# Kernel tuning notes

Measured on AMD Instinct MI355X. Metric: run time of the kernel, lower is better.

Reference implementation:

```python
import jax, jax.numpy as jnp
import numpy as np

V, D, H, L, T_CTX = 50257, 768, 12, 12, 1024
HD = D // H
GELU_C = float(np.sqrt(2.0 / np.pi))


def new_gelu(x):
    return 0.5 * x * (1.0 + jnp.tanh(GELU_C * (x + 0.044715 * x ** 3)))


def layernorm(x, w, b, eps=1e-5):
    mu = jnp.mean(x, axis=-1, keepdims=True)
    var = jnp.var(x, axis=-1, keepdims=True)
    return (x - mu) * jax.lax.rsqrt(var + eps) * w + b


def setup_inputs() -> dict:
    key = jax.random.key(0)
    ks = jax.random.split(key, 20)
    B, T = 2, 1024
    s = 0.02
    inp = {
        "idx": jax.random.randint(ks[0], (B, T), 0, V),
        "targets": jax.random.randint(ks[1], (B, T), 0, V),
        "wte": jax.random.normal(ks[2], (V, D), jnp.float32) * s,
        "wpe": jax.random.normal(ks[3], (T_CTX, D), jnp.float32) * s,
        "ln1_w": jnp.ones((L, D)), "ln1_b": jnp.zeros((L, D)),
        "qkv_w": jax.random.normal(ks[4], (L, D, 3 * D), jnp.float32) * s,
        "qkv_b": jnp.zeros((L, 3 * D)),
        "proj_w": jax.random.normal(ks[5], (L, D, D), jnp.float32) * s,
        "proj_b": jnp.zeros((L, D)),
        "ln2_w": jnp.ones((L, D)), "ln2_b": jnp.zeros((L, D)),
        "fc_w": jax.random.normal(ks[6], (L, D, 4 * D), jnp.float32) * s,
        "fc_b": jnp.zeros((L, 4 * D)),
        "fc2_w": jax.random.normal(ks[7], (L, 4 * D, D), jnp.float32) * s,
        "fc2_b": jnp.zeros((L, D)),
        "lnf_w": jnp.ones((D,)), "lnf_b": jnp.zeros((D,)),
    }
    return inp


def _gpt_forward(idx, targets, wte, wpe, ln1_w, ln1_b, qkv_w, qkv_b, proj_w,
                 proj_b, ln2_w, ln2_b, fc_w, fc_b, fc2_w, fc2_b, lnf_w, lnf_b):
    B, T = idx.shape
    x = wte[idx] + wpe[:T]  # [B,T,D]
    scale = 1.0 / np.sqrt(HD)
    causal = jnp.tril(jnp.ones((T, T), dtype=bool))

    def block(x, p):
        l1w, l1b, qw, qb, pw, pb, l2w, l2b, fw, fb, f2w, f2b = p
        h = layernorm(x, l1w, l1b)
        qkv = h @ qw + qb  # [B,T,3D]
        q, k, v = jnp.split(qkv, 3, axis=-1)
        q = q.reshape(B, T, H, HD).transpose(0, 2, 1, 3)
        k = k.reshape(B, T, H, HD).transpose(0, 2, 1, 3)
        v = v.reshape(B, T, H, HD).transpose(0, 2, 1, 3)
        attn = jnp.einsum('bhqd,bhkd->bhqk', q, k) * scale
        attn = jnp.where(causal, attn, -jnp.inf)
        attn = jax.nn.softmax(attn, axis=-1)
        o = jnp.einsum('bhqk,bhkd->bhqd', attn, v)
        o = o.transpose(0, 2, 1, 3).reshape(B, T, D)
        x = x + (o @ pw + pb)
        h = layernorm(x, l2w, l2b)
        h = new_gelu(h @ fw + fb) @ f2w + f2b
        return x + h, None

    params = (ln1_w, ln1_b, qkv_w, qkv_b, proj_w, proj_b,
              ln2_w, ln2_b, fc_w, fc_b, fc2_w, fc2_b)
    x, _ = jax.lax.scan(block, x, params)
    x = layernorm(x, lnf_w, lnf_b)
    logits = x @ wte.T  # tied lm_head, [B,T,V]

    logp = jax.nn.log_softmax(logits, axis=-1)
    tflat = targets.reshape(-1)
    valid = tflat != -1
    tsafe = jnp.where(valid, tflat, 0)
    nll = -jnp.take_along_axis(logp.reshape(-1, V), tsafe[:, None], axis=-1)[:, 0]
    loss = jnp.sum(jnp.where(valid, nll, 0.0)) / jnp.maximum(jnp.sum(valid), 1)
    return logits, loss


def reference(idx, targets, wte, wpe, ln1_w, ln1_b, qkv_w, qkv_b, proj_w,
              proj_b, ln2_w, ln2_b, fc_w, fc_b, fc2_w, fc2_b, lnf_w, lnf_b):
    return _gpt_forward(idx, targets, wte, wpe, ln1_w, ln1_b, qkv_w, qkv_b,
                        proj_w, proj_b, ln2_w, ln2_b, fc_w, fc_b, fc2_w, fc2_b,
                        lnf_w, lnf_b)
```

## Files before the change

kernel.cpp:

```cpp
#include <hip/hip_runtime.h>
#include <hip/hip_bf16.h>
#include <math.h>

#define TT 1024
#define BB 2
#define DD 768
#define HH 12
#define NHD 64
#define LL 12
#define VV 50257
#define MROWS (BB*TT)
#define VPAD 50304

typedef __attribute__((ext_vector_type(4))) float f32x4;
typedef __attribute__((ext_vector_type(8))) __bf16 bf16x8;
typedef __attribute__((ext_vector_type(8))) unsigned short u16x8;
typedef __hip_bfloat16 bf16;

__device__ __forceinline__ void gload_lds16(const bf16* g, bf16* l) {
    __builtin_amdgcn_global_load_lds((const __attribute__((address_space(1))) void*)g,
                                     (__attribute__((address_space(3))) void*)l, 16, 0, 0);
}

__global__ void embed_kernel(const int* __restrict__ idx, const float* __restrict__ wte,
                             const float* __restrict__ wpe, float* __restrict__ x) {
    int m = blockIdx.x;
    int t = m % TT;
    int tok = idx[m];
    const float* wrow = wte + (size_t)tok * DD;
    const float* prow = wpe + (size_t)t * DD;
    float* xrow = x + (size_t)m * DD;
    for (int c = threadIdx.x; c < DD; c += blockDim.x)
        xrow[c] = wrow[c] + prow[c];
}

__global__ void ln_kernel(const float* __restrict__ x, const float* __restrict__ w,
                          const float* __restrict__ b, bf16* __restrict__ out) {
    __shared__ float red[256];
    int m = blockIdx.x;
    int tid = threadIdx.x;
    const float* xr = x + (size_t)m * DD;
    float v0 = xr[tid], v1 = xr[tid + 256], v2 = xr[tid + 512];
    red[tid] = v0 + v1 + v2;
    __syncthreads();
    for (int s = 128; s > 0; s >>= 1) { if (tid < s) red[tid] += red[tid + s]; __syncthreads(); }
    float mu = red[0] * (1.0f / DD);
    __syncthreads();
    float d0 = v0 - mu, d1 = v1 - mu, d2 = v2 - mu;
    red[tid] = d0 * d0 + d1 * d1 + d2 * d2;
    __syncthreads();
    for (int s = 128; s > 0; s >>= 1) { if (tid < s) red[tid] += red[tid + s]; __syncthreads(); }
    float rstd = rsqrtf(red[0] * (1.0f / DD) + 1e-5f);
    bf16* orow = out + (size_t)m * DD;
    orow[tid]       = __float2bfloat16(d0 * rstd * w[tid]       + b[tid]);
    orow[tid + 256] = __float2bfloat16(d1 * rstd * w[tid + 256] + b[tid + 256]);
    orow[tid + 512] = __float2bfloat16(d2 * rstd * w[tid + 512] + b[tid + 512]);
}

__global__ void cast_kernel(const float* __restrict__ src, bf16* __restrict__ dst, int n4) {
    int stride = gridDim.x * blockDim.x;
    for (int i = blockIdx.x * blockDim.x + threadIdx.x; i < n4; i += stride) {
        float4 v = *(const float4*)(src + (size_t)i * 4);
        bf16* d = dst + (size_t)i * 4;
        d[0] = __float2bfloat16(v.x); d[1] = __float2bfloat16(v.y);
        d[2] = __float2bfloat16(v.z); d[3] = __float2bfloat16(v.w);
    }
}

__global__ void tcast_kernel(const float* __restrict__ W, bf16* __restrict__ Wt,
                             int K, int N, size_t wstride, size_t tstride) {
    W  += (size_t)blockIdx.z * wstride;
    Wt += (size_t)blockIdx.z * tstride;
    __shared__ float t[32][33];
    int n0 = blockIdx.x * 32, k0 = blockIdx.y * 32;
    int c = threadIdx.x & 31, g = threadIdx.x >> 5;
    #pragma unroll
    for (int i = 0; i < 4; ++i) {
        int k = g * 4 + i;
        t[k][c] = W[(size_t)(k0 + k) * N + n0 + c];
    }
    __syncthreads();
    #pragma unroll
    for (int i = 0; i < 4; ++i) {
        int n = g * 4 + i;
        Wt[(size_t)(n0 + n) * K + k0 + c] = __float2bfloat16(t[c][n]);
    }
}

template<int BM, int BN, bool BIAS, bool GELU_, bool RES, bool OUTBF16, bool NCHECK, bool SPLITK>
__global__ __launch_bounds__(256, 3) void mgemm(
        const bf16* __restrict__ A, const bf16* __restrict__ Bm,
        const float* __restrict__ bias, const float* __restrict__ res,
        float* __restrict__ Cf, bf16* __restrict__ Cb, int M, int N, int K) {
    constexpr int WM = BM / 32, WN = BN / 32;
    constexpr int RA = BM / 64, RB = BN / 64;
    constexpr int NL = RA + RB;
    __shared__ __align__(16) bf16 As[2][BM * 32];
    __shared__ __align__(16) bf16 Bs[2][BN * 32];
    const int tid = threadIdx.x, lane = tid & 63, wid = tid >> 6;
    const int nbx = gridDim.x;
    const int nwg = nbx * gridDim.y;
    const int bidl = blockIdx.x + nbx * blockIdx.y;
    const int cpx = nwg >> 3;
    const int sw = (bidl & 7) * cpx + (bidl >> 3);
    const int m0 = (sw % nbx) * BM, n0 = (sw / nbx) * BN;
    const int wr = (wid >> 1) * (BM / 2), wc = (wid & 1) * (BN / 2);
    const int fr = lane & 15, fq = lane >> 4;

    const int Keff  = SPLITK ? (K >> 1) : K;
    const int kbase = SPLITK ? blockIdx.z * Keff : 0;
    if (SPLITK) Cf += (size_t)blockIdx.z * M * N;

    const int ksrc = ((lane & 3) ^ ((lane >> 3) & 3)) * 8;
    const bf16* gA = A  + (size_t)(m0 + wid * 16 + (lane >> 2)) * K + kbase + ksrc;
    const bf16* gB = Bm + (size_t)(n0 + wid * 16 + (lane >> 2)) * K + kbase + ksrc;
    bf16* lA = &As[0][0] + wid * 512 + lane * 8;
    bf16* lB = &Bs[0][0] + wid * 512 + lane * 8;
    const int kph = (fq ^ ((fr >> 1) & 3)) * 8;

    f32x4 acc[WM][WN] = {};
    const int nt = Keff / 32;

    #pragma unroll
    for (int i = 0; i < RA; ++i) gload_lds16(gA + (size_t)(i * 64) * K, lA + i * 2048);
    #pragma unroll
    for (int i = 0; i < RB; ++i) gload_lds16(gB + (size_t)(i * 64) * K, lB + i * 2048);

    for (int t = 0; t < nt; ++t) {
        const int cur = t & 1;
        if (t + 1 < nt) {
            const bf16* pA = gA + (t + 1) * 32;
            const bf16* pB = gB + (t + 1) * 32;
            bf16* dA = lA + (cur ^ 1) * (BM * 32);
            bf16* dB = lB + (cur ^ 1) * (BN * 32);
            #pragma unroll
            for (int i = 0; i < RA; ++i) gload_lds16(pA + (size_t)(i * 64) * K, dA + i * 2048);
            #pragma unroll
            for (int i = 0; i < RB; ++i) gload_lds16(pB + (size_t)(i * 64) * K, dB + i * 2048);
            asm volatile("s_waitcnt vmcnt(%0)" :: "i"(NL) : "memory");
        } else {
            asm volatile("s_waitcnt vmcnt(0)" ::: "memory");
        }
        __builtin_amdgcn_s_barrier();
        __builtin_amdgcn_sched_barrier(0);
        const bf16* abase = &As[cur][0];
        const bf16* bbase = &Bs[cur][0];
        bf16x8 af[WM], bq[WN];
        #pragma unroll
        for (int m = 0; m < WM; ++m)
            af[m] = *(const bf16x8*)(abase + (wr + m * 16 + fr) * 32 + kph);
        #pragma unroll
        for (int n = 0; n < WN; ++n)
            bq[n] = *(const bf16x8*)(bbase + (wc + n * 16 + fr) * 32 + kph);
        #pragma unroll
        for (int m = 0; m < WM; ++m)
            #pragma unroll
            for (int n = 0; n < WN; ++n)
                acc[m][n] = __builtin_amdgcn_mfma_f32_16x16x32_bf16(af[m], bq[n], acc[m][n], 0, 0, 0);
        __builtin_amdgcn_sched_barrier(0);
        __builtin_amdgcn_s_barrier();
    }

    #pragma unroll
    for (int m = 0; m < WM; ++m) {
        const int row = m0 + wr + m * 16 + fq * 4;
        #pragma unroll
        for (int n = 0; n < WN; ++n) {
            const int col = n0 + wc + n * 16 + fr;
            if (NCHECK && col >= N) continue;
            float bv = BIAS ? bias[col] : 0.f;
            #pragma unroll
            for (int r = 0; r < 4; ++r) {
                float v = acc[m][n][r] + bv;
                if (GELU_) {
                    float u = v;
                    v = 0.5f * u * (1.0f + tanhf(0.7978845608028654f * (u + 0.044715f * u * u * u)));
                }
                if (RES) v += res[(size_t)(row + r) * N + col];
                if (OUTBF16) Cb[(size_t)(row + r) * N + col] = __float2bfloat16(v);
                else         Cf[(size_t)(row + r) * N + col] = v;
            }
        }
    }
}

__global__ void red_kernel(const float* __restrict__ part, const float* __restrict__ bias,
                           float* __restrict__ x) {
    const size_t MN = (size_t)MROWS * DD;
    size_t i = ((size_t)blockIdx.x * blockDim.x + threadIdx.x) * 4;
    float4 p0 = *(const float4*)(part + i);
    float4 p1 = *(const float4*)(part + MN + i);
    float4 xv = *(const float4*)(x + i);
    float4 bv = *(const float4*)(bias + (int)(i % DD));
    xv.x += p0.x + p1.x + bv.x;
    xv.y += p0.y + p1.y + bv.y;
    xv.z += p0.z + p1.z + bv.z;
    xv.w += p0.w + p1.w + bv.w;
    *(float4*)(x + i) = xv;
}

__global__ __launch_bounds__(256) void attn3_kernel(const bf16* __restrict__ qkv,
                                                    bf16* __restrict__ out) {
    __shared__ bf16 Vt[64 * 64];
    __shared__ bf16 Ps[4][16 * 64];
    const int bid = blockIdx.x;
    const int q0 = (15 - (bid & 15)) * 64;
    const int h  = (bid / (TT / 64)) % HH;
    const int b  = bid / ((TT / 64) * HH);
    const int tid = threadIdx.x, lane = tid & 63, wid = tid >> 6;
    const int fr = lane & 15, fq = lane >> 4;
    const size_t rs = 3 * DD;

    bf16x8 qf[2];
    {
        const bf16* qb = qkv + (size_t)(b * TT + q0 + wid * 16 + fr) * rs + h * NHD;
        qf[0] = *(const bf16x8*)(qb + fq * 8);
        qf[1] = *(const bf16x8*)(qb + 32 + fq * 8);
    }
    float mrun[4] = {-1e30f, -1e30f, -1e30f, -1e30f};
    float lrun[4] = {0.f, 0.f, 0.f, 0.f};
    f32x4 o[4] = {};
    const int vrow = (tid & 31) * 2, kq = tid >> 5;
    const int ntile = q0 / 64 + 1;

    for (int jt = 0; jt < ntile; ++jt) {
        __syncthreads();
        {
            const u16x8* vb = (const u16x8*)(qkv + (size_t)(b * TT + jt * 64 + vrow) * rs + 2 * DD + h * NHD + kq * 8);
            u16x8 v0 = vb[0];
            u16x8 v1 = *(const u16x8*)((const bf16*)vb + rs);
            #pragma unroll
            for (int j = 0; j < 8; ++j) {
                int d = kq * 8 + j;
                int e = (d * 64 + vrow) ^ ((d & 7) << 3);
                *(unsigned int*)&Vt[e] = (unsigned int)v0[j] | ((unsigned int)v1[j] << 16);
            }
        }
        f32x4 s[4] = {};
        const bf16* kb = qkv + (size_t)(b * TT + jt * 64 + fr) * rs + DD + h * NHD;
        __builtin_amdgcn_s_setprio(1);
        #pragma unroll
        for (int n = 0; n < 4; ++n) {
            bf16x8 k0 = *(const bf16x8*)(kb + (size_t)(n * 16) * rs + fq * 8);
            bf16x8 k1 = *(const bf16x8*)(kb + (size_t)(n * 16) * rs + 32 + fq * 8);
            s[n] = __builtin_amdgcn_mfma_f32_16x16x32_bf16(qf[0], k0, s[n], 0, 0, 0);
            s[n] = __builtin_amdgcn_mfma_f32_16x16x32_bf16(qf[1], k1, s[n], 0, 0, 0);
        }
        __builtin_amdgcn_s_setprio(0);
        float mt[4] = {-1e30f, -1e30f, -1e30f, -1e30f};
        #pragma unroll
        for (int n = 0; n < 4; ++n) {
            int colg = jt * 64 + n * 16 + fr;
            #pragma unroll
            for (int r = 0; r < 4; ++r) {
                int rowg = q0 + wid * 16 + fq * 4 + r;
                float v = s[n][r] * 0.125f;
                if (colg > rowg) v = -1e30f;
                s[n][r] = v;
                mt[r] = fmaxf(mt[r], v);
            }
        }
        #pragma unroll
        for (int msk = 1; msk <= 8; msk <<= 1)
            #pragma unroll
            for (int r = 0; r < 4; ++r) mt[r] = fmaxf(mt[r], __shfl_xor(mt[r], msk));
        float sc[4], pt[4] = {0.f, 0.f, 0.f, 0.f};
        #pragma unroll
        for (int r = 0; r < 4; ++r) {
            float mn = fmaxf(mrun[r], mt[r]);
            sc[r] = __expf(mrun[r] - mn);
            mrun[r] = mn;
        }
        #pragma unroll
        for (int n = 0; n < 4; ++n)
            #pragma unroll
            for (int r = 0; r < 4; ++r) {
                float p = __expf(s[n][r] - mrun[r]);
                s[n][r] = p;
                pt[r] += p;
            }
        #pragma unroll
        for (int msk = 1; msk <= 8; msk <<= 1)
            #pragma unroll
            for (int r = 0; r < 4; ++r) pt[r] += __shfl_xor(pt[r], msk);
        #pragma unroll
        for (int r = 0; r < 4; ++r) lrun[r] = lrun[r] * sc[r] + pt[r];
        #pragma unroll
        for (int n2 = 0; n2 < 4; ++n2)
            #pragma unroll
            for (int r = 0; r < 4; ++r) o[n2][r] *= sc[r];
        #pragma unroll
        for (int n = 0; n < 4; ++n)
            #pragma unroll
            for (int r = 0; r < 4; ++r) {
                int row = fq * 4 + r;
                int e = (row * 64 + n * 16 + fr) ^ ((row & 7) << 3);
                Ps[wid][e] = __float2bfloat16(s[n][r]);
            }
        __syncthreads();
        __builtin_amdgcn_s_setprio(1);
        #pragma unroll
        for (int ks = 0; ks < 2; ++ks) {
            int pe = (fr * 64 + ks * 32 + fq * 8) ^ ((fr & 7) << 3);
            bf16x8 pa = *(const bf16x8*)&Ps[wid][pe];
            #pragma unroll
            for (int n2 = 0; n2 < 4; ++n2) {
                int d = n2 * 16 + fr;
                int ve = (d * 64 + ks * 32 + fq * 8) ^ ((d & 7) << 3);
                bf16x8 vv = *(const bf16x8*)&Vt[ve];
                o[n2] = __builtin_amdgcn_mfma_f32_16x16x32_bf16(pa, vv, o[n2], 0, 0, 0);
            }
        }
        __builtin_amdgcn_s_setprio(0);
    }
    #pragma unroll
    for (int r = 0; r < 4; ++r) {
        float inv = 1.f / lrun[r];
        bf16* op = out + (size_t)(b * TT + q0 + wid * 16 + fq * 4 + r) * DD + h * NHD;
        #pragma unroll
        for (int n2 = 0; n2 < 4; ++n2)
            op[n2 * 16 + fr] = __float2bfloat16(o[n2][r] * inv);
    }
}

__global__ void zero_kernel(float* p) { if (threadIdx.x == 0) p[0] = 0.f; }

__device__ __forceinline__ void ol_push(float v, float& mx, float& sm) {
    if (v > mx) { sm *= __expf(mx - v); mx = v; }
    sm += __expf(v - mx);
}

__global__ void loss_kernel(const float* __restrict__ logits, const int* __restrict__ targets,
                            float* __restrict__ acc) {
    __shared__ float rm[256], rs[256];
    int m = blockIdx.x;
    int tid = threadIdx.x;
    const float* lr = logits + (size_t)m * VV;
    const int lead = (4 - (m & 3)) & 3;
    const int nv = (VV - lead) >> 2;
    float mx = -1e30f, sm = 0.f;
    if (tid < lead) ol_push(lr[tid], mx, sm);
    const float4* lr4 = (const float4*)(lr + lead);
    for (int i = tid; i < nv; i += 256) {
        float4 v = lr4[i];
        ol_push(v.x, mx, sm); ol_push(v.y, mx, sm);
        ol_push(v.z, mx, sm); ol_push(v.w, mx, sm);
    }
    for (int i = lead + 4 * nv + tid; i < VV; i += 256) ol_push(lr[i], mx, sm);
    rm[tid] = mx; rs[tid] = sm;
    __syncthreads();
    for (int s = 128; s > 0; s >>= 1) {
        if (tid < s) {
            float m2 = rm[tid + s], s2 = rs[tid + s];
            float nm = fmaxf(rm[tid], m2);
            rs[tid] = rs[tid] * __expf(rm[tid] - nm) + s2 * __expf(m2 - nm);
            rm[tid] = nm;
        }
        __syncthreads();
    }
    if (tid == 0) {
        float lse = logf(rs[0]) + rm[0];
        atomicAdd(acc, lse - lr[targets[m]]);
    }
}

__global__ void loss_final(const float* __restrict__ acc, float* __restrict__ out) {
    if (threadIdx.x == 0) out[0] = acc[0] * (1.0f / (float)MROWS);
}

extern "C" void kernel_launch(void* const* d_in, const int* in_sizes, int n_in,
                              void* d_out, int out_size, void* d_ws, size_t ws_size,
                              hipStream_t stream) {
    const int*   idx     = (const int*)d_in[0];
    const int*   targets = (const int*)d_in[1];
    const float* wte     = (const float*)d_in[2];
    const float* wpe     = (const float*)d_in[3];
    const float* ln1_w   = (const float*)d_in[4];
    const float* ln1_b   = (const float*)d_in[5];
    const float* qkv_w   = (const float*)d_in[6];
    const float* qkv_b   = (const float*)d_in[7];
    const float* proj_w  = (const float*)d_in[8];
    const float* proj_b  = (const float*)d_in[9];
    const float* ln2_w   = (const float*)d_in[10];
    const float* ln2_b   = (const float*)d_in[11];
    const float* fc_w    = (const float*)d_in[12];
    const float* fc_b    = (const float*)d_in[13];
    const float* fc2_w   = (const float*)d_in[14];
    const float* fc2_b   = (const float*)d_in[15];
    const float* lnf_w   = (const float*)d_in[16];
    const float* lnf_b   = (const float*)d_in[17];

    float* logits = (float*)d_out;
    float* loss_out = logits + (size_t)MROWS * VV;

    const size_t LQ = (size_t)3 * DD * DD, LP = (size_t)DD * DD;
    const size_t LF = (size_t)4 * DD * DD, LF2 = (size_t)4 * DD * DD;
    const size_t LSTRIDE = LQ + LP + LF + LF2;

    float* x    = (float*)d_ws;
    float* lacc = x + (size_t)MROWS * DD;
    float* part = lacc + 16;
    bf16* qkvbuf = (bf16*)(part + (size_t)2 * MROWS * DD);
    bf16* hb   = qkvbuf + (size_t)MROWS * 3 * DD;
    bf16* ab   = hb + (size_t)MROWS * DD;
    bf16* gb   = ab + (size_t)MROWS * DD;
    bf16* wteb = gb + (size_t)MROWS * 4 * DD;
    bf16* wbase = wteb + (size_t)VPAD * DD;

    const size_t fixed_bytes = (size_t)((char*)wbase - (char*)d_ws);
    const bool hoist = ws_size >= fixed_bytes + sizeof(bf16) * LSTRIDE * LL;

    dim3 blk(256);
    cast_kernel<<<2048, blk, 0, stream>>>(wte, wteb, VV * DD / 4);
    embed_kernel<<<MROWS, blk, 0, stream>>>(idx, wte, wpe, x);

    if (hoist) {
        tcast_kernel<<<dim3(3 * DD / 32, DD / 32, LL), blk, 0, stream>>>(
            qkv_w, wbase, DD, 3 * DD, LQ, LSTRIDE);
        tcast_kernel<<<dim3(DD / 32, DD / 32, LL), blk, 0, stream>>>(
            proj_w, wbase + LQ, DD, DD, LP, LSTRIDE);
        tcast_kernel<<<dim3(4 * DD / 32, DD / 32, LL), blk, 0, stream>>>(
            fc_w, wbase + LQ + LP, DD, 4 * DD, LF, LSTRIDE);
        tcast_kernel<<<dim3(DD / 32, 4 * DD / 32, LL), blk, 0, stream>>>(
            fc2_w, wbase + LQ + LP + LF, 4 * DD, DD, LF2, LSTRIDE);
    }

    const int nred = (MROWS * DD) / (4 * 256);

    for (int l = 0; l < LL; ++l) {
        bf16* wl = hoist ? wbase + (size_t)l * LSTRIDE : wbase;
        bf16* wQT = wl, *wPT = wl + LQ, *wFT = wl + LQ + LP, *wF2T = wl + LQ + LP + LF;
        if (!hoist) {
            tcast_kernel<<<dim3(3 * DD / 32, DD / 32, 1), blk, 0, stream>>>(qkv_w + (size_t)l * LQ, wQT, DD, 3 * DD, 0, 0);
            tcast_kernel<<<dim3(DD / 32, DD / 32, 1), blk, 0, stream>>>(proj_w + (size_t)l * LP, wPT, DD, DD, 0, 0);
            tcast_kernel<<<dim3(4 * DD / 32, DD / 32, 1), blk, 0, stream>>>(fc_w + (size_t)l * LF, wFT, DD, 4 * DD, 0, 0);
            tcast_kernel<<<dim3(DD / 32, 4 * DD / 32, 1), blk, 0, stream>>>(fc2_w + (size_t)l * LF2, wF2T, 4 * DD, DD, 0, 0);
        }

        ln_kernel<<<MROWS, blk, 0, stream>>>(x, ln1_w + (size_t)l * DD, ln1_b + (size_t)l * DD, hb);

        mgemm<128, 128, true, false, false, true, false, false><<<dim3(MROWS / 128, 3 * DD / 128), blk, 0, stream>>>(
            hb, wQT, qkv_b + (size_t)l * 3 * DD, nullptr, nullptr, qkvbuf, MROWS, 3 * DD, DD);

        attn3_kernel<<<BB * HH * (TT / 64), blk, 0, stream>>>(qkvbuf, ab);

        mgemm<64, 64, false, false, false, false, false, true><<<dim3(MROWS / 64, DD / 64, 2), blk, 0, stream>>>(
            ab, wPT, nullptr, nullptr, part, nullptr, MROWS, DD, DD);
        red_kernel<<<nred, blk, 0, stream>>>(part, proj_b + (size_t)l * DD, x);

        ln_kernel<<<MROWS, blk, 0, stream>>>(x, ln2_w + (size_t)l * DD, ln2_b + (size_t)l * DD, hb);

        mgemm<128, 128, true, true, false, true, false, false><<<dim3(MROWS / 128, 4 * DD / 128), blk, 0, stream>>>(
            hb, wFT, fc_b + (size_t)l * 4 * DD, nullptr, nullptr, gb, MROWS, 4 * DD, DD);

        mgemm<64, 64, false, false, false, false, false, true><<<dim3(MROWS / 64, DD / 64, 2), blk, 0, stream>>>(
            gb, wF2T, nullptr, nullptr, part, nullptr, MROWS, DD, 4 * DD);
        red_kernel<<<nred, blk, 0, stream>>>(part, fc2_b + (size_t)l * DD, x);
    }

    ln_kernel<<<MROWS, blk, 0, stream>>>(x, lnf_w, lnf_b, hb);

    mgemm<128, 128, false, false, false, false, true, false><<<dim3(MROWS / 128, VPAD / 128), blk, 0, stream>>>(
        hb, wteb, nullptr, nullptr, logits, nullptr, MROWS, VV, DD);

    zero_kernel<<<1, 64, 0, stream>>>(lacc);
    loss_kernel<<<MROWS, blk, 0, stream>>>(logits, targets, lacc);
    loss_final<<<1, 64, 0, stream>>>(lacc, loss_out);
}
```

Before: 2.567 ms.

## Fuse residual reduction with layernorm, fuse logsumexp into lm_head GEMM, retune tiles

Merges the split-K reduction and residual add with the following layernorm into one redln kernel, removing separate ln/red launches and one pass over x. Adds a dedicated lm_head GEMM that writes logits with nontemporal stores and emits per-tile (max, sumexp) partials, so the loss kernel no longer rereads the full 2048x50257 logits. It also zero-pads the padded wte rows so the N check can be dropped, rewrites GELU as x*sigmoid(2z) using __expf, and changes the QKV and FC tile shapes. The result is more launches-saved fusion in exchange for extra code and slightly different GELU rounding.

After: 2.508 ms. 1.02x faster.

```diff
diff --git a/kernel.cpp b/kernel.cpp
--- a/kernel.cpp
+++ b/kernel.cpp
@@ -11,6 +11,7 @@
 #define VV 50257
 #define MROWS (BB*TT)
 #define VPAD 50304
+#define NT 393
 
 typedef __attribute__((ext_vector_type(4))) float f32x4;
 typedef __attribute__((ext_vector_type(8))) __bf16 bf16x8;
@@ -57,6 +58,37 @@
     orow[tid + 512] = __float2bfloat16(d2 * rstd * w[tid + 512] + b[tid + 512]);
 }
 
+__global__ void redln_kernel(const float* __restrict__ part, const float* __restrict__ bias,
+                             const float* __restrict__ w, const float* __restrict__ b,
+                             float* __restrict__ x, bf16* __restrict__ hb) {
+    __shared__ float red[256];
+    const size_t MN = (size_t)MROWS * DD;
+    int m = blockIdx.x;
+    int tid = threadIdx.x;
+    float v[3];
+    #pragma unroll
+    for (int j = 0; j < 3; ++j) {
+        int c = tid + j * 256;
+        size_t i = (size_t)m * DD + c;
+        v[j] = x[i] + part[i] + part[MN + i] + bias[c];
+        x[i] = v[j];
+    }
+    red[tid] = v[0] + v[1] + v[2];
+    __syncthreads();
+    for (int s = 128; s > 0; s >>= 1) { if (tid < s) red[tid] += red[tid + s]; __syncthreads(); }
+    float mu = red[0] * (1.0f / DD);
+    __syncthreads();
+    float d0 = v[0] - mu, d1 = v[1] - mu, d2 = v[2] - mu;
+    red[tid] = d0 * d0 + d1 * d1 + d2 * d2;
+    __syncthreads();
+    for (int s = 128; s > 0; s >>= 1) { if (tid < s) red[tid] += red[tid + s]; __syncthreads(); }
+    float rstd = rsqrtf(red[0] * (1.0f / DD) + 1e-5f);
+    bf16* orow = hb + (size_t)m * DD;
+    orow[tid]       = __float2bfloat16(d0 * rstd * w[tid]       + b[tid]);
+    orow[tid + 256] = __float2bfloat16(d1 * rstd * w[tid + 256] + b[tid + 256]);
+    orow[tid + 512] = __float2bfloat16(d2 * rstd * w[tid + 512] + b[tid + 512]);
+}
+
 __global__ void cast_kernel(const float* __restrict__ src, bf16* __restrict__ dst, int n4) {
     int stride = gridDim.x * blockDim.x;
     for (int i = blockIdx.x * blockDim.x + threadIdx.x; i < n4; i += stride) {
@@ -67,6 +99,11 @@
     }
 }
 
+__global__ void padzero_kernel(bf16* __restrict__ p, int n) {
+    int i = blockIdx.x * 256 + threadIdx.x;
+    if (i < n) p[i] = __float2bfloat16(0.f);
+}
+
 __global__ void tcast_kernel(const float* __restrict__ W, bf16* __restrict__ Wt,
                              int K, int N, size_t wstride, size_t tstride) {
     W  += (size_t)blockIdx.z * wstride;
@@ -87,7 +124,7 @@
     }
 }
 
-template<int BM, int BN, bool BIAS, bool GELU_, bool RES, bool OUTBF16, bool NCHECK, bool SPLITK>
+template<int BM, int BN, bool BIAS, bool GELU_, bool RES, bool OUTBF16, bool SPLITK>
 __global__ __launch_bounds__(256, 3) void mgemm(
         const bf16* __restrict__ A, const bf16* __restrict__ Bm,
         const float* __restrict__ bias, const float* __restrict__ res,
@@ -167,14 +204,14 @@
         #pragma unroll
         for (int n = 0; n < WN; ++n) {
             const int col = n0 + wc + n * 16 + fr;
-            if (NCHECK && col >= N) continue;
             float bv = BIAS ? bias[col] : 0.f;
             #pragma unroll
             for (int r = 0; r < 4; ++r) {
                 float v = acc[m][n][r] + bv;
                 if (GELU_) {
                     float u = v;
-                    v = 0.5f * u * (1.0f + tanhf(0.7978845608028654f * (u + 0.044715f * u * u * u)));
+                    float z = 1.5957691216057308f * (u + 0.044715f * u * u * u);
+                    v = u / (1.0f + __expf(-z));
                 }
                 if (RES) v += res[(size_t)(row + r) * N + col];
                 if (OUTBF16) Cb[(size_t)(row + r) * N + col] = __float2bfloat16(v);
@@ -184,20 +221,120 @@
     }
 }
 
-__global__ void red_kernel(const float* __restrict__ part, const float* __restrict__ bias,
-                           float* __restrict__ x) {
-    const size_t MN = (size_t)MROWS * DD;
-    size_t i = ((size_t)blockIdx.x * blockDim.x + threadIdx.x) * 4;
-    float4 p0 = *(const float4*)(part + i);
-    float4 p1 = *(const float4*)(part + MN + i);
-    float4 xv = *(const float4*)(x + i);
-    float4 bv = *(const float4*)(bias + (int)(i % DD));
-    xv.x += p0.x + p1.x + bv.x;
-    xv.y += p0.y + p1.y + bv.y;
-    xv.z += p0.z + p1.z + bv.z;
-    xv.w += p0.w + p1.w + bv.w;
-    *(float4*)(x + i) = xv;
-}
+__global__ __launch_bounds__(256, 3) void mgemmL(
+        const bf16* __restrict__ A, const bf16* __restrict__ Bm,
+        float* __restrict__ Cf, float2* __restrict__ P, int N, int K) {
+    constexpr int NL = 4;
+    __shared__ __align__(16) bf16 As[2][128 * 32];
+    __shared__ __align__(16) bf16 Bs[2][128 * 32];
+    __shared__ float2 lbuf[4][64];
+    const int tid = threadIdx.x, lane = tid & 63, wid = tid >> 6;
+    const int nbx = gridDim.x;
+    const int nwg = nbx * gridDim.y;
+    const int bidl = blockIdx.x + nbx * blockIdx.y;
+    const int cpx = nwg >> 3;
+    const int sw = (bidl & 7) * cpx + (bidl >> 3);
+    const int m0 = (sw % nbx) * 128, n0 = (sw / nbx) * 128;
+    const int wr = (wid >> 1) * 64, wc = (wid & 1) * 64;
+    const int fr = lane & 15, fq = lane >> 4;
+
+    const int ksrc = ((lane & 3) ^ ((lane >> 3) & 3)) * 8;
+    const bf16* gA = A  + (size_t)(m0 + wid * 16 + (lane >> 2)) * K + ksrc;
+    const bf16* gB = Bm + (size_t)(n0 + wid * 16 + (lane >> 2)) * K + ksrc;
+    bf16* lA = &As[0][0] + wid * 512 + lane * 8;
+    bf16* lB = &Bs[0][0] + wid * 512 + lane * 8;
+    const int kph = (fq ^ ((fr >> 1) & 3)) * 8;
+
+    f32x4 acc[4][4] = {};
+    const int nt = K / 32;
+
+    #pragma unroll
+    for (int i = 0; i < 2; ++i) gload_lds16(gA + (size_t)(i * 64) * K, lA + i * 2048);
+    #pragma unroll
+    for (int i = 0; i < 2; ++i) gload_lds16(gB + (size_t)(i * 64) * K, lB + i * 2048);
+
+    for (int t = 0; t < nt; ++t) {
+        const int cur = t & 1;
+        if (t + 1 < nt) {
+            const bf16* pA = gA + (t + 1) * 32;
+            const bf16* pB = gB + (t + 1) * 32;
+            bf16* dA = lA + (cur ^ 1) * (128 * 32);
+            bf16* dB = lB + (cur ^ 1) * (128 * 32);
+            #pragma unroll
+            for (int i = 0; i < 2; ++i) gload_lds16(pA + (size_t)(i * 64) * K, dA + i * 2048);
+            #pragma unroll
+            for (int i = 0; i < 2; ++i) gload_lds16(pB + (size_t)(i * 64) * K, dB + i * 2048);
+            asm volatile("s_waitcnt vmcnt(%0)" :: "i"(NL) : "memory");
+        } else {
+            asm volatile("s_waitcnt vmcnt(0)" ::: "memory");
+        }
+        __builtin_amdgcn_s_barrier();
+        __builtin_amdgcn_sched_barrier(0);
+        const bf16* abase = &As[cur][0];
+        const bf16* bbase = &Bs[cur][0];
+        bf16x8 af[4], bq[4];
+        #pragma unroll
+        for (int m = 0; m < 4; ++m)
+            af[m] = *(const bf16x8*)(abase + (wr + m * 16 + fr) * 32 + kph);
+        #pragma unroll
+        for (int n = 0; n < 4; ++n)
+            bq[n] = *(const bf16x8*)(bbase + (wc + n * 16 + fr) * 32 + kph);
+        #pragma unroll
+        for (int m = 0; m < 4; ++m)
+            #pragma unroll
+            for (int n = 0; n < 4; ++n)
+                acc[m][n] = __builtin_amdgcn_mfma_f32_16x16x32_bf16(af[m], bq[n], acc[m][n], 0, 0, 0);
+        __builtin_amdgcn_sched_barrier(0);
+        __builtin_amdgcn_s_barrier();
+    }
+
+    #pragma unroll
+    for (int m = 0; m < 4; ++m) {
+        const int row = m0 + wr + m * 16 + fq * 4;
+        #pragma unroll
+        for (int n = 0; n < 4; ++n) {
+            const int col = n0 + wc + n * 16 + fr;
+            if (col < N) {
+                #pragma unroll
+                for (int r = 0; r < 4; ++r)
+                    __builtin_nontemporal_store(acc[m][n][r], &Cf[(size_t)(row + r) * N + col]);
+            }
+        }
+    }
+    #pragma unroll
+    for (int m = 0; m < 4; ++m) {
+        #pragma unroll
+        for (int r = 0; r < 4; ++r) {
+            float mx = -1e30f;
+            #pragma unroll
+            for (int n = 0; n < 4; ++n) {
+                int col = n0 + wc + n * 16 + fr;
+                mx = fmaxf(mx, (col < N) ? acc[m][n][r] : -1e30f);
+            }
+            #pragma unroll
+            for (int msk = 1; msk <= 8; msk <<= 1) mx = fmaxf(mx, __shfl_xor(mx, msk));
+            float sm = 0.f;
+            #pragma unroll
+            for (int n = 0; n < 4; ++n) {
+                int col = n0 + wc + n * 16 + fr;
+                if (col < N) sm += __expf(acc[m][n][r] - mx);
+            }
+            #pragma unroll
+            for (int msk = 1; msk <= 8; msk <<= 1) sm += __shfl_xor(sm, msk);
+            if (fr == 0) lbuf[wid][m * 16 + fq * 4 + r] = make_float2(mx, sm);
+        }
+    }
+    __syncthreads();
+    if (tid < 128) {
+        int half = tid >> 6, rl = tid & 63;
+        float2 a = lbuf[half * 2][rl];
+        float2 b = lbuf[half * 2 + 1][rl];
+        float mc = fmaxf(a.x, b.x);
+        float sc = a.y * __expf(a.x - mc) + b.y * __expf(b.x - mc);
+        P[(size_t)(m0 + half * 64 + rl) * NT + (n0 >> 7)] = make_float2(mc, sc);
+    }
+}
+
 
 __global__ __launch_bounds__(256) void attn3_kernel(const bf16* __restrict__ qkv,
                                                     bf16* __restrict__ out) {
@@ -325,28 +462,18 @@
 
 __global__ void zero_kernel(float* p) { if (threadIdx.x == 0) p[0] = 0.f; }
 
-__device__ __forceinline__ void ol_push(float v, float& mx, float& sm) {
-    if (v > mx) { sm *= __expf(mx - v); mx = v; }
-    sm += __expf(v - mx);
-}
-
-__global__ void loss_kernel(const float* __restrict__ logits, const int* __restrict__ targets,
-                            float* __restrict__ acc) {
+__global__ void loss_finish(const float2* __restrict__ P, const float* __restrict__ logits,
+                            const int* __restrict__ targets, float* __restrict__ acc) {
     __shared__ float rm[256], rs[256];
     int m = blockIdx.x;
     int tid = threadIdx.x;
-    const float* lr = logits + (size_t)m * VV;
-    const int lead = (4 - (m & 3)) & 3;
-    const int nv = (VV - lead) >> 2;
     float mx = -1e30f, sm = 0.f;
-    if (tid < lead) ol_push(lr[tid], mx, sm);
-    const float4* lr4 = (const float4*)(lr + lead);
-    for (int i = tid; i < nv; i += 256) {
-        float4 v = lr4[i];
-        ol_push(v.x, mx, sm); ol_push(v.y, mx, sm);
-        ol_push(v.z, mx, sm); ol_push(v.w, mx, sm);
-    }
-    for (int i = lead + 4 * nv + tid; i < VV; i += 256) ol_push(lr[i], mx, sm);
+    for (int i = tid; i < NT; i += 256) {
+        float2 p = P[(size_t)m * NT + i];
+        float nm = fmaxf(mx, p.x);
+        sm = sm * __expf(mx - nm) + p.y * __expf(p.x - nm);
+        mx = nm;
+    }
     rm[tid] = mx; rs[tid] = sm;
     __syncthreads();
     for (int s = 128; s > 0; s >>= 1) {
@@ -360,7 +487,7 @@
     }
     if (tid == 0) {
         float lse = logf(rs[0]) + rm[0];
-        atomicAdd(acc, lse - lr[targets[m]]);
+        atomicAdd(acc, lse - logits[(size_t)m * VV + targets[m]]);
     }
 }
 
@@ -412,6 +539,8 @@
 
     dim3 blk(256);
     cast_kernel<<<2048, blk, 0, stream>>>(wte, wteb, VV * DD / 4);
+    padzero_kernel<<<((VPAD - VV) * DD + 255) / 256, blk, 0, stream>>>(
+        wteb + (size_t)VV * DD, (VPAD - VV) * DD);
     embed_kernel<<<MROWS, blk, 0, stream>>>(idx, wte, wpe, x);
 
     if (hoist) {
@@ -425,7 +554,7 @@
             fc2_w, wbase + LQ + LP + LF, 4 * DD, DD, LF2, LSTRIDE);
     }
 
-    const int nred = (MROWS * DD) / (4 * 256);
+    ln_kernel<<<MROWS, blk, 0, stream>>>(x, ln1_w, ln1_b, hb);
 
     for (int l = 0; l < LL; ++l) {
         bf16* wl = hoist ? wbase + (size_t)l * LSTRIDE : wbase;
@@ -437,33 +566,30 @@
             tcast_kernel<<<dim3(DD / 32, 4 * DD / 32, 1), blk, 0, stream>>>(fc2_w + (size_t)l * LF2, wF2T, 4 * DD, DD, 0, 0);
         }
 
-        ln_kernel<<<MROWS, blk, 0, stream>>>(x, ln1_w + (size_t)l * DD, ln1_b + (size_t)l * DD, hb);
-
-        mgemm<128, 128, true, false, false, true, false, false><<<dim3(MROWS / 128, 3 * DD / 128), blk, 0, stream>>>(
+        mgemm<64, 64, true, false, false, true, false><<<dim3(MROWS / 64, 3 * DD / 64), blk, 0, stream>>>(
             hb, wQT, qkv_b + (size_t)l * 3 * DD, nullptr, nullptr, qkvbuf, MROWS, 3 * DD, DD);
 
         attn3_kernel<<<BB * HH * (TT / 64), blk, 0, stream>>>(qkvbuf, ab);
 
-        mgemm<64, 64, false, false, false, false, false, true><<<dim3(MROWS / 64, DD / 64, 2), blk, 0, stream>>>(
+        mgemm<64, 64, false, false, false, false, true><<<dim3(MROWS / 64, DD / 64, 2), blk, 0, stream>>>(
             ab, wPT, nullptr, nullptr, part, nullptr, MROWS, DD, DD);
-        red_kernel<<<nred, blk, 0, stream>>>(part, proj_b + (size_t)l * DD, x);
-
-        ln_kernel<<<MROWS, blk, 0, stream>>>(x, ln2_w + (size_t)l * DD, ln2_b + (size_t)l * DD, hb);
-
-        mgemm<128, 128, true, true, false, true, false, false><<<dim3(MROWS / 128, 4 * DD / 128), blk, 0, stream>>>(
+        redln_kernel<<<MROWS, blk, 0, stream>>>(part, proj_b + (size_t)l * DD,
+            ln2_w + (size_t)l * DD, ln2_b + (size_t)l * DD, x, hb);
+
+        mgemm<128, 64, true, true, false, true, false><<<dim3(MROWS / 128, 4 * DD / 64), blk, 0, stream>>>(
             hb, wFT, fc_b + (size_t)l * 4 * DD, nullptr, nullptr, gb, MROWS, 4 * DD, DD);
 
-        mgemm<64, 64, false, false, false, false, false, true><<<dim3(MROWS / 64, DD / 64, 2), blk, 0, stream>>>(
+        mgemm<64, 64, false, false, false, false, true><<<dim3(MROWS / 64, DD / 64, 2), blk, 0, stream>>>(
             gb, wF2T, nullptr, nullptr, part, nullptr, MROWS, DD, 4 * DD);
-        red_kernel<<<nred, blk, 0, stream>>>(part, fc2_b + (size_t)l * DD, x);
-    }
-
-    ln_kernel<<<MROWS, blk, 0, stream>>>(x, lnf_w, lnf_b, hb);
-
-    mgemm<128, 128, false, false, false, false, true, false><<<dim3(MROWS / 128, VPAD / 128), blk, 0, stream>>>(
-        hb, wteb, nullptr, nullptr, logits, nullptr, MROWS, VV, DD);
+        const float* nw = (l + 1 < LL) ? ln1_w + (size_t)(l + 1) * DD : lnf_w;
+        const float* nb = (l + 1 < LL) ? ln1_b + (size_t)(l + 1) * DD : lnf_b;
+        redln_kernel<<<MROWS, blk, 0, stream>>>(part, fc2_b + (size_t)l * DD, nw, nb, x, hb);
+    }
+
+    mgemmL<<<dim3(MROWS / 128, VPAD / 128), blk, 0, stream>>>(
+        hb, wteb, logits, (float2*)part, VV, DD);
 
     zero_kernel<<<1, 64, 0, stream>>>(lacc);
-    loss_kernel<<<MROWS, blk, 0, stream>>>(logits, targets, lacc);
+    loss_finish<<<MROWS, blk, 0, stream>>>((const float2*)part, logits, targets, lacc);
     loss_final<<<1, 64, 0, stream>>>(lacc, loss_out);
 }
```
